# Performance work log

Hardware: AMD Instinct MI355X
Metric: run time of the kernel (lower is better)

Reference implementation:

```python
import jax, jax.numpy as jnp
import numpy as np

B, S, H = 8, 4096, 1152
LENGTH = 256


def setup_inputs() -> dict:
    key = jax.random.key(0)
    k1, k2 = jax.random.split(key)
    hidden_states = jax.random.normal(k1, (B, S, H), dtype=jnp.float32)
    # (x, y) patch coordinates on a 64x64 grid
    patch_positions = jax.random.randint(k2, (B, S, 2), 0, 64, dtype=jnp.int64)
    padding_positions = jnp.ones((B, LENGTH), dtype=jnp.bool_)
    return {
        "hidden_states": hidden_states,
        "patch_positions": patch_positions,
        "padding_positions": padding_positions,
    }


def _pool(hidden_states, patch_positions, length):
    b, s, h = hidden_states.shape
    k = int((s // length) ** 0.5)
    k_sq = k * k
    assert k_sq * length == s
    clamped = jnp.maximum(patch_positions, 0)  # clamp(min=0)
    max_x = jnp.max(clamped[..., 0], axis=-1, keepdims=True) + 1  # [B,1]
    kidx = clamped // k
    kernel_idxs = kidx[..., 0] + (max_x // k) * kidx[..., 1]  # [B,S], values < length
    # segment-mean instead of the one-hot GEMM: identical math
    seg = (kernel_idxs + length * jnp.arange(b, dtype=kernel_idxs.dtype)[:, None]).reshape(-1)
    pooled = jax.ops.segment_sum(
        hidden_states.reshape(b * s, h), seg, num_segments=b * length
    ).reshape(b, length, h) / k_sq
    counts = jax.ops.segment_sum(
        jnp.ones((b * s,), dtype=jnp.int32), seg, num_segments=b * length
    ).reshape(b, length)
    mask = counts > 0  # equivalent to ~(weights == 0).all(dim=1)
    return pooled, mask


def reference(hidden_states, patch_positions, padding_positions):
    length = LENGTH
    if hidden_states.shape[1] == length:
        pooled, mask = hidden_states, padding_positions
    else:
        pooled, mask = _pool(hidden_states, patch_positions, length)
    root_hidden_size = float(hidden_states.shape[-1]) ** 0.5
    pooled = pooled * root_hidden_size
    return pooled, mask
```

## Files before the change

### kernel.cpp

```cpp
#include <hip/hip_runtime.h>
#include <hip/hip_bf16.h>

#define NB 8
#define NS 4096
#define NH 1152
#define LEN 256
#define KK 4
#define F4ROW (NH / 4)

#define WS_COUNTS 0
#define WS_STARTS 2048
#define WS_ORDER  4096

__global__ void gvp_prep(const int* __restrict__ patch, int* __restrict__ ws,
                         float* __restrict__ maskout) {
    int b = blockIdx.x;
    int t = threadIdx.x;
    __shared__ int s_seg[NS];
    __shared__ int s_cnt[LEN];
    __shared__ int s_cur[LEN];
    __shared__ int sd[LEN];
    __shared__ int s_max[4];
    __shared__ int s_mult;

    const int2* p2 = (const int2*)(patch + (size_t)b * NS * 2);
    int xs[16], ys[16];
    int m = 0;
    #pragma unroll
    for (int i = 0; i < 16; ++i) {
        int s = t + 256 * i;
        int2 v = p2[s];
        int x = v.x < 0 ? 0 : v.x;
        int y = v.y < 0 ? 0 : v.y;
        xs[i] = x; ys[i] = y;
        m = max(m, x);
    }
    #pragma unroll
    for (int off = 32; off > 0; off >>= 1)
        m = max(m, __shfl_down(m, off, 64));
    if ((t & 63) == 0) s_max[t >> 6] = m;
    s_cnt[t] = 0;
    __syncthreads();
    if (t == 0) {
        int mm = max(max(s_max[0], s_max[1]), max(s_max[2], s_max[3]));
        s_mult = (mm + 1) >> 2;
    }
    __syncthreads();
    int mult = s_mult;

    #pragma unroll
    for (int i = 0; i < 16; ++i) {
        int seg = (xs[i] >> 2) + mult * (ys[i] >> 2);
        if (seg > LEN - 1) seg = LEN - 1;
        s_seg[t + 256 * i] = seg;
        atomicAdd(&s_cnt[seg], 1);
    }
    __syncthreads();

    int c = s_cnt[t];
    sd[t] = c;
    __syncthreads();
    for (int off = 1; off < 256; off <<= 1) {
        int v = (t >= off) ? sd[t - off] : 0;
        __syncthreads();
        sd[t] += v;
        __syncthreads();
    }
    int base = sd[t] - c;
    s_cur[t] = base;
    ws[WS_STARTS + b * LEN + t] = b * NS + base;
    ws[WS_COUNTS + b * LEN + t] = c;
    maskout[b * LEN + t] = (c > 0) ? 1.0f : 0.0f;
    __syncthreads();

    #pragma unroll
    for (int i = 0; i < 16; ++i) {
        int s = t + 256 * i;
        int pos = atomicAdd(&s_cur[s_seg[s]], 1);
        ws[WS_ORDER + b * NS + pos] = s;
    }
}

__global__ void gvp_gather(const float* __restrict__ hidden,
                           const int* __restrict__ ws,
                           float* __restrict__ out) {
    __shared__ int rows[NS];
    int g = blockIdx.x;
    int b = g >> 8;
    int t = threadIdx.x;
    int start = ws[WS_STARTS + g];
    int cnt   = ws[WS_COUNTS + g];
    for (int i = t; i < cnt; i += 256) rows[i] = ws[WS_ORDER + start + i];
    __syncthreads();

    float4 a0 = make_float4(0.f, 0.f, 0.f, 0.f);
    float4 a1 = make_float4(0.f, 0.f, 0.f, 0.f);
    float4 b0 = make_float4(0.f, 0.f, 0.f, 0.f);
    float4 b1 = make_float4(0.f, 0.f, 0.f, 0.f);
    const float* hb = hidden + (size_t)b * NS * NH;
    int r = 0;
    for (; r + 1 < cnt; r += 2) {
        const float4* rowA = (const float4*)(hb + (size_t)rows[r] * NH);
        const float4* rowB = (const float4*)(hb + (size_t)rows[r + 1] * NH);
        float4 vA = rowA[t];
        float4 vB = rowB[t];
        a0.x += vA.x; a0.y += vA.y; a0.z += vA.z; a0.w += vA.w;
        b0.x += vB.x; b0.y += vB.y; b0.z += vB.z; b0.w += vB.w;
        if (t < F4ROW - 256) {
            float4 wA = rowA[t + 256];
            float4 wB = rowB[t + 256];
            a1.x += wA.x; a1.y += wA.y; a1.z += wA.z; a1.w += wA.w;
            b1.x += wB.x; b1.y += wB.y; b1.z += wB.z; b1.w += wB.w;
        }
    }
    if (r < cnt) {
        const float4* rowA = (const float4*)(hb + (size_t)rows[r] * NH);
        float4 vA = rowA[t];
        a0.x += vA.x; a0.y += vA.y; a0.z += vA.z; a0.w += vA.w;
        if (t < F4ROW - 256) {
            float4 wA = rowA[t + 256];
            a1.x += wA.x; a1.y += wA.y; a1.z += wA.z; a1.w += wA.w;
        }
    }
    a0.x += b0.x; a0.y += b0.y; a0.z += b0.z; a0.w += b0.w;
    a1.x += b1.x; a1.y += b1.y; a1.z += b1.z; a1.w += b1.w;

    const float scale = 2.1213203435596424f;
    float4* og = (float4*)(out + (size_t)g * NH);
    og[t] = make_float4(a0.x * scale, a0.y * scale, a0.z * scale, a0.w * scale);
    if (t < F4ROW - 256)
        og[t + 256] = make_float4(a1.x * scale, a1.y * scale, a1.z * scale, a1.w * scale);
}

extern "C" void kernel_launch(void* const* d_in, const int* in_sizes, int n_in,
                              void* d_out, int out_size, void* d_ws, size_t ws_size,
                              hipStream_t stream) {
    const float* hidden = (const float*)d_in[0];
    const int*   patch  = (const int*)d_in[1];
    float* out = (float*)d_out;
    float* maskout = out + (size_t)NB * LEN * NH;
    int* ws = (int*)d_ws;

    gvp_prep  <<<NB,       256, 0, stream>>>(patch, ws, maskout);
    gvp_gather<<<NB * LEN, 256, 0, stream>>>(hidden, ws, out);
}
```

Before: 38.29 us.

## Fuse segment-index prep into gather kernel, each block selecting its own rows

Replaces the two-kernel design (a per-batch counting/prefix-scan/scatter prep kernel plus a gather kernel) with one kernel. Each block recomputes segment ids for all 4096 positions of its batch and keeps only the rows that match its own segment, collecting them in shared memory with an atomic counter. This removes a launch, the workspace round trip and the serial 8-block prep stage. In exchange, every block redundantly re-reads the batch's patch coordinates, about 32KB per block. The accumulation loop is also unrolled to four rows per iteration, and the clamp of segment ids to 255 is dropped.

```diff
diff --git a/kernel.cpp b/kernel.cpp
--- a/kernel.cpp
+++ b/kernel.cpp
@@ -5,131 +5,95 @@
 #define NS 4096
 #define NH 1152
 #define LEN 256
-#define KK 4
 #define F4ROW (NH / 4)
 
-#define WS_COUNTS 0
-#define WS_STARTS 2048
-#define WS_ORDER  4096
+__global__ void gvp_fused(const float* __restrict__ hidden,
+                          const int* __restrict__ patch,
+                          float* __restrict__ out,
+                          float* __restrict__ maskout) {
+    int g = blockIdx.x;
+    int b = g >> 8;
+    int myseg = g & (LEN - 1);
+    int t = threadIdx.x;
 
-__global__ void gvp_prep(const int* __restrict__ patch, int* __restrict__ ws,
-                         float* __restrict__ maskout) {
-    int b = blockIdx.x;
-    int t = threadIdx.x;
-    __shared__ int s_seg[NS];
-    __shared__ int s_cnt[LEN];
-    __shared__ int s_cur[LEN];
-    __shared__ int sd[LEN];
+    __shared__ int rows[NS];
     __shared__ int s_max[4];
+    __shared__ int s_cnt;
     __shared__ int s_mult;
+    if (t == 0) s_cnt = 0;
 
     const int2* p2 = (const int2*)(patch + (size_t)b * NS * 2);
-    int xs[16], ys[16];
+    int pk[16];
     int m = 0;
     #pragma unroll
     for (int i = 0; i < 16; ++i) {
-        int s = t + 256 * i;
-        int2 v = p2[s];
+        int2 v = p2[t + 256 * i];
         int x = v.x < 0 ? 0 : v.x;
         int y = v.y < 0 ? 0 : v.y;
-        xs[i] = x; ys[i] = y;
+        pk[i] = x | (y << 16);
         m = max(m, x);
     }
     #pragma unroll
     for (int off = 32; off > 0; off >>= 1)
         m = max(m, __shfl_down(m, off, 64));
     if ((t & 63) == 0) s_max[t >> 6] = m;
-    s_cnt[t] = 0;
     __syncthreads();
-    if (t == 0) {
-        int mm = max(max(s_max[0], s_max[1]), max(s_max[2], s_max[3]));
-        s_mult = (mm + 1) >> 2;
-    }
+    if (t == 0)
+        s_mult = (max(max(s_max[0], s_max[1]), max(s_max[2], s_max[3])) + 1) >> 2;
     __syncthreads();
     int mult = s_mult;
 
     #pragma unroll
     for (int i = 0; i < 16; ++i) {
-        int seg = (xs[i] >> 2) + mult * (ys[i] >> 2);
-        if (seg > LEN - 1) seg = LEN - 1;
-        s_seg[t + 256 * i] = seg;
-        atomicAdd(&s_cnt[seg], 1);
+        int x = pk[i] & 0xffff;
+        int y = pk[i] >> 16;
+        int seg = (x >> 2) + mult * (y >> 2);
+        if (seg == myseg) {
+            int pos = atomicAdd(&s_cnt, 1);
+            rows[pos] = t + 256 * i;
+        }
     }
     __syncthreads();
-
-    int c = s_cnt[t];
-    sd[t] = c;
-    __syncthreads();
-    for (int off = 1; off < 256; off <<= 1) {
-        int v = (t >= off) ? sd[t - off] : 0;
-        __syncthreads();
-        sd[t] += v;
-        __syncthreads();
-    }
-    int base = sd[t] - c;
-    s_cur[t] = base;
-    ws[WS_STARTS + b * LEN + t] = b * NS + base;
-    ws[WS_COUNTS + b * LEN + t] = c;
-    maskout[b * LEN + t] = (c > 0) ? 1.0f : 0.0f;
-    __syncthreads();
-
-    #pragma unroll
-    for (int i = 0; i < 16; ++i) {
-        int s = t + 256 * i;
-        int pos = atomicAdd(&s_cur[s_seg[s]], 1);
-        ws[WS_ORDER + b * NS + pos] = s;
-    }
-}
-
-__global__ void gvp_gather(const float* __restrict__ hidden,
-                           const int* __restrict__ ws,
-                           float* __restrict__ out) {
-    __shared__ int rows[NS];
-    int g = blockIdx.x;
-    int b = g >> 8;
-    int t = threadIdx.x;
-    int start = ws[WS_STARTS + g];
-    int cnt   = ws[WS_COUNTS + g];
-    for (int i = t; i < cnt; i += 256) rows[i] = ws[WS_ORDER + start + i];
-    __syncthreads();
+    int cnt = s_cnt;
 
     float4 a0 = make_float4(0.f, 0.f, 0.f, 0.f);
     float4 a1 = make_float4(0.f, 0.f, 0.f, 0.f);
-    float4 b0 = make_float4(0.f, 0.f, 0.f, 0.f);
-    float4 b1 = make_float4(0.f, 0.f, 0.f, 0.f);
+    float4 c0 = make_float4(0.f, 0.f, 0.f, 0.f);
+    float4 c1 = make_float4(0.f, 0.f, 0.f, 0.f);
     const float* hb = hidden + (size_t)b * NS * NH;
     int r = 0;
-    for (; r + 1 < cnt; r += 2) {
-        const float4* rowA = (const float4*)(hb + (size_t)rows[r] * NH);
-        const float4* rowB = (const float4*)(hb + (size_t)rows[r + 1] * NH);
-        float4 vA = rowA[t];
-        float4 vB = rowB[t];
-        a0.x += vA.x; a0.y += vA.y; a0.z += vA.z; a0.w += vA.w;
-        b0.x += vB.x; b0.y += vB.y; b0.z += vB.z; b0.w += vB.w;
+    for (; r + 3 < cnt; r += 4) {
+        const float4* rA = (const float4*)(hb + (size_t)rows[r]     * NH);
+        const float4* rB = (const float4*)(hb + (size_t)rows[r + 1] * NH);
+        const float4* rC = (const float4*)(hb + (size_t)rows[r + 2] * NH);
+        const float4* rD = (const float4*)(hb + (size_t)rows[r + 3] * NH);
+        float4 vA = rA[t], vB = rB[t], vC = rC[t], vD = rD[t];
+        a0.x += vA.x + vB.x; a0.y += vA.y + vB.y; a0.z += vA.z + vB.z; a0.w += vA.w + vB.w;
+        c0.x += vC.x + vD.x; c0.y += vC.y + vD.y; c0.z += vC.z + vD.z; c0.w += vC.w + vD.w;
         if (t < F4ROW - 256) {
-            float4 wA = rowA[t + 256];
-            float4 wB = rowB[t + 256];
-            a1.x += wA.x; a1.y += wA.y; a1.z += wA.z; a1.w += wA.w;
-            b1.x += wB.x; b1.y += wB.y; b1.z += wB.z; b1.w += wB.w;
+            float4 wA = rA[t + 256], wB = rB[t + 256], wC = rC[t + 256], wD = rD[t + 256];
+            a1.x += wA.x + wB.x; a1.y += wA.y + wB.y; a1.z += wA.z + wB.z; a1.w += wA.w + wB.w;
+            c1.x += wC.x + wD.x; c1.y += wC.y + wD.y; c1.z += wC.z + wD.z; c1.w += wC.w + wD.w;
         }
     }
-    if (r < cnt) {
-        const float4* rowA = (const float4*)(hb + (size_t)rows[r] * NH);
-        float4 vA = rowA[t];
+    for (; r < cnt; ++r) {
+        const float4* rA = (const float4*)(hb + (size_t)rows[r] * NH);
+        float4 vA = rA[t];
         a0.x += vA.x; a0.y += vA.y; a0.z += vA.z; a0.w += vA.w;
         if (t < F4ROW - 256) {
-            float4 wA = rowA[t + 256];
+            float4 wA = rA[t + 256];
             a1.x += wA.x; a1.y += wA.y; a1.z += wA.z; a1.w += wA.w;
         }
     }
-    a0.x += b0.x; a0.y += b0.y; a0.z += b0.z; a0.w += b0.w;
-    a1.x += b1.x; a1.y += b1.y; a1.z += b1.z; a1.w += b1.w;
+    a0.x += c0.x; a0.y += c0.y; a0.z += c0.z; a0.w += c0.w;
+    a1.x += c1.x; a1.y += c1.y; a1.z += c1.z; a1.w += c1.w;
 
     const float scale = 2.1213203435596424f;
     float4* og = (float4*)(out + (size_t)g * NH);
     og[t] = make_float4(a0.x * scale, a0.y * scale, a0.z * scale, a0.w * scale);
     if (t < F4ROW - 256)
         og[t + 256] = make_float4(a1.x * scale, a1.y * scale, a1.z * scale, a1.w * scale);
+    if (t == 0) maskout[g] = (cnt > 0) ? 1.0f : 0.0f;
 }
 
 extern "C" void kernel_launch(void* const* d_in, const int* in_sizes, int n_in,
@@ -139,8 +103,6 @@
     const int*   patch  = (const int*)d_in[1];
     float* out = (float*)d_out;
     float* maskout = out + (size_t)NB * LEN * NH;
-    int* ws = (int*)d_ws;
 
-    gvp_prep  <<<NB,       256, 0, stream>>>(patch, ws, maskout);
-    gvp_gather<<<NB * LEN, 256, 0, stream>>>(hidden, ws, out);
+    gvp_fused<<<NB * LEN, 256, 0, stream>>>(hidden, patch, out, maskout);
 }
```

After: 31.86 us. -16.8%, faster.
